# Kernel optimization log

Hardware: AMD Instinct MI355X
Metric: run time of the kernel (lower is better)

The kernel has to match this reference:

```python
import jax, jax.numpy as jnp
import numpy as np

DIM = 512
HEADS = 8
HEAD_DIM = 64
RS = 16        # region_size
EPEG_K = 15
L_TOKENS = 36864  # 192^2, multiple of RS^2 grid


def setup_inputs() -> dict:
    key = jax.random.key(0)
    ks = jax.random.split(key, 5)
    s = 1.0 / np.sqrt(DIM)
    x = jax.random.normal(ks[0], (1, L_TOKENS, DIM), jnp.float32)
    W_qkv = jax.random.normal(ks[1], (3 * HEADS * HEAD_DIM, DIM), jnp.float32) * s
    b_qkv = jnp.zeros((3 * HEADS * HEAD_DIM,), jnp.float32)
    W_proj = jax.random.normal(ks[2], (DIM, HEADS * HEAD_DIM), jnp.float32) * s
    b_proj = jnp.zeros((DIM,), jnp.float32)
    pe_w = jax.random.normal(ks[3], (HEADS, 1, EPEG_K, 1), jnp.float32) * 0.05
    pe_b = jnp.zeros((HEADS,), jnp.float32)
    return dict(x=x, W_qkv=W_qkv, b_qkv=b_qkv, W_proj=W_proj, b_proj=b_proj,
                pe_w=pe_w, pe_b=pe_b)


def reference(x, W_qkv, b_qkv, W_proj, b_proj, pe_w, pe_b):
    B, L, C = x.shape
    # --- padding() logic: square to HxW, H multiple of region_size ---
    H = int(np.ceil(np.sqrt(L)))
    H += (-H) % RS
    W = H
    add = H * W - L
    if add > 0:
        x = jnp.concatenate([x, jnp.zeros((B, add, C), x.dtype)], axis=1)
    # --- region_partition: (B,H,W,C) -> (num_regions*B, RS*RS, C) ---
    xr = (x.reshape(B, H // RS, RS, W // RS, RS, C)
            .transpose(0, 1, 3, 2, 4, 5)
            .reshape(-1, RS * RS, C))
    B_, N, _ = xr.shape
    # --- InnerAttention ---
    qkv = xr @ W_qkv.T + b_qkv                       # (B_, N, 3*h*d)
    qkv = qkv.reshape(B_, N, 3, HEADS, HEAD_DIM).transpose(2, 0, 3, 1, 4)
    q, k, v = qkv[0], qkv[1], qkv[2]                 # each (B_, h, N, d)
    scale = HEAD_DIM ** -0.5
    attn = jnp.einsum('bhid,bhjd->bhij', q * scale, k)   # (B_, h, N, N)
    # EPEG: depthwise conv (k,1) over the query axis of the score map
    pad = EPEG_K // 2
    pe = jax.lax.conv_general_dilated(
        attn, pe_w, window_strides=(1, 1), padding=((pad, pad), (0, 0)),
        dimension_numbers=('NCHW', 'OIHW', 'NCHW'), feature_group_count=HEADS)
    pe = pe + pe_b[None, :, None, None]
    attn = jax.nn.softmax(attn + pe, axis=-1)
    out = jnp.einsum('bhij,bhjd->bhid', attn, v)     # (B_, h, N, d)
    out = out.transpose(0, 2, 1, 3).reshape(B_, N, HEADS * HEAD_DIM)
    out = out @ W_proj.T + b_proj                    # (B_, N, C)
    # --- region_reverse ---
    out = (out.reshape(B, H // RS, W // RS, RS, RS, C)
              .transpose(0, 1, 3, 2, 4, 5)
              .reshape(B, H * W, C))
    if add > 0:
        out = out[:, :L]
    return out
```

## Files before the change

kernel.cpp:

```cpp
#include <hip/hip_runtime.h>
#include <stdint.h>

typedef __attribute__((ext_vector_type(8))) __bf16 bf16x8;
typedef __attribute__((ext_vector_type(16))) float f32x16;

__device__ __forceinline__ unsigned short f2bf(float f) {
  union { float f; unsigned int u; } v;
  v.f = f;
  unsigned int u = v.u;
  return (unsigned short)((u + 0x7FFFu + ((u >> 16) & 1u)) >> 16);
}

union BFrag { unsigned short u[8]; unsigned int w[4]; bf16x8 v; };

__device__ __forceinline__ f32x16 mfma32(bf16x8 a, bf16x8 b, f32x16 c) {
  return __builtin_amdgcn_mfma_f32_32x32x16_bf16(a, b, c, 0, 0, 0);
}

#define GLOAD_LDS16(gptr, lptr)                                                \
  __builtin_amdgcn_global_load_lds(                                           \
      (const __attribute__((address_space(1))) void*)(gptr),                  \
      (__attribute__((address_space(3))) void*)(lptr), 16, 0, 0)

__global__ __launch_bounds__(256) void k_xgather(const float* __restrict__ x,
                                                 unsigned short* __restrict__ xb) {
  int idx = blockIdx.x * 256 + threadIdx.x;
  int m = idx >> 6;
  int seg = (idx & 63) << 3;
  int r = m >> 8, n = m & 255;
  int a = r / 12, b = r - a * 12;
  int ii = n >> 4, jj = n & 15;
  long g = (long)((a * 16 + ii) * 192 + b * 16 + jj);
  const float4* p = (const float4*)(x + g * 512 + seg);
  float4 v0 = p[0], v1 = p[1];
  union { unsigned short u[8]; int4 v; } o;
  o.u[0] = f2bf(v0.x); o.u[1] = f2bf(v0.y); o.u[2] = f2bf(v0.z); o.u[3] = f2bf(v0.w);
  o.u[4] = f2bf(v1.x); o.u[5] = f2bf(v1.y); o.u[6] = f2bf(v1.z); o.u[7] = f2bf(v1.w);
  *(int4*)(xb + (size_t)m * 512 + seg) = o.v;
}

__global__ __launch_bounds__(256) void k_cvt(const float* __restrict__ s,
                                             unsigned short* __restrict__ d, int n8) {
  int i = blockIdx.x * 256 + threadIdx.x;
  if (i >= n8) return;
  const float4* p = (const float4*)(s + (size_t)i * 8);
  float4 a = p[0], b = p[1];
  union { unsigned short u[8]; int4 v; } o;
  o.u[0] = f2bf(a.x); o.u[1] = f2bf(a.y); o.u[2] = f2bf(a.z); o.u[3] = f2bf(a.w);
  o.u[4] = f2bf(b.x); o.u[5] = f2bf(b.y); o.u[6] = f2bf(b.z); o.u[7] = f2bf(b.w);
  *(int4*)(d + (size_t)i * 8) = o.v;
}

template<int MODE, int NBN>
__global__ __launch_bounds__(256, 2) void k_gemm(
    const unsigned short* __restrict__ A, const unsigned short* __restrict__ B,
    const float* __restrict__ bias,
    unsigned short* __restrict__ qb, unsigned short* __restrict__ kb,
    unsigned short* __restrict__ vtb, float* __restrict__ out) {
  __shared__ unsigned short As[8192];
  __shared__ unsigned short Bs[8192];
  int t = threadIdx.x;
  constexpr int NWG = NBN * 288;
  int d0 = blockIdx.x;
  int tl = (d0 & 7) * (NWG >> 3) + (d0 >> 3);
  int bm = tl / NBN, bn = tl % NBN;

  int w = t >> 6, lane = t & 63;
  int l31 = lane & 31, lh = lane >> 5;
  int wr = w >> 1, wc = w & 1;

  int srow = t >> 3, cseg = t & 7;
  int csw = (cseg ^ (srow & 7)) << 3;
  int ldsWaveOff = (t >> 6) << 10;

  f32x16 acc[2][2];
  for (int i = 0; i < 2; ++i)
    for (int j = 0; j < 2; ++j)
      for (int e = 0; e < 16; ++e) acc[i][j][e] = 0.0f;

  const unsigned short* Ag = A + (size_t)(bm * 128 + srow) * 512 + csw;
  const unsigned short* Bg = B + (size_t)(bn * 128 + srow) * 512 + csw;

  for (int ks = 0; ks < 8; ++ks) {
#pragma unroll
    for (int rnd = 0; rnd < 4; ++rnd) {
      GLOAD_LDS16(Ag + (size_t)rnd * 32 * 512 + ks * 64,
                  (char*)As + ldsWaveOff + rnd * 4096);
      GLOAD_LDS16(Bg + (size_t)rnd * 32 * 512 + ks * 64,
                  (char*)Bs + ldsWaveOff + rnd * 4096);
    }
    __syncthreads();
#pragma unroll
    for (int kt = 0; kt < 4; ++kt) {
      bf16x8 af[2], bfr[2];
#pragma unroll
      for (int mt = 0; mt < 2; ++mt) {
        int r = wr * 64 + mt * 32 + l31;
        af[mt] = *(const bf16x8*)((const char*)As + r * 128 +
                                  ((kt * 32 + lh * 16) ^ ((r & 7) << 4)));
      }
#pragma unroll
      for (int nt = 0; nt < 2; ++nt) {
        int r = wc * 64 + nt * 32 + l31;
        bfr[nt] = *(const bf16x8*)((const char*)Bs + r * 128 +
                                   ((kt * 32 + lh * 16) ^ ((r & 7) << 4)));
      }
#pragma unroll
      for (int mt = 0; mt < 2; ++mt)
#pragma unroll
        for (int nt = 0; nt < 2; ++nt)
          acc[mt][nt] = mfma32(af[mt], bfr[nt], acc[mt][nt]);
    }
    __syncthreads();
  }

  int nBase = bn * 128 + wc * 64;
  int mBase = bm * 128 + wr * 64;
#pragma unroll
  for (int nt = 0; nt < 2; ++nt) {
    int nn = nBase + nt * 32 + l31;
    float bs = bias[nn];
    if (MODE == 0) {
      int tsel = nn >> 9, rem = nn & 511;
      int hh = rem >> 6, d = rem & 63;
#pragma unroll
      for (int mt = 0; mt < 2; ++mt) {
#pragma unroll
        for (int q = 0; q < 4; ++q) {
          int m0 = mBase + mt * 32 + q * 8 + lh * 4;
          int r = m0 >> 8, tok = m0 & 255;
          size_t base = (size_t)(r * 8 + hh) * 16384;
          if (tsel == 0) {
#pragma unroll
            for (int j = 0; j < 4; ++j)
              qb[base + (size_t)(tok + j) * 64 + d] = f2bf((acc[mt][nt][q * 4 + j] + bs) * 0.125f);
          } else if (tsel == 1) {
#pragma unroll
            for (int j = 0; j < 4; ++j)
              kb[base + (size_t)(tok + j) * 64 + d] = f2bf(acc[mt][nt][q * 4 + j] + bs);
          } else {
            unsigned long long pv = 0;
#pragma unroll
            for (int j = 0; j < 4; ++j)
              pv |= (unsigned long long)f2bf(acc[mt][nt][q * 4 + j] + bs) << (16 * j);
            *(unsigned long long*)(vtb + base + (size_t)d * 256 + tok) = pv;
          }
        }
      }
    } else {
#pragma unroll
      for (int mt = 0; mt < 2; ++mt) {
#pragma unroll
        for (int q = 0; q < 4; ++q) {
          int m0 = mBase + mt * 32 + q * 8 + lh * 4;
          int r = m0 >> 8;
          int a = r / 12, bcol = r - a * 12;
#pragma unroll
          for (int j = 0; j < 4; ++j) {
            int tok = (m0 & 255) + j;
            int ii = tok >> 4, jj = tok & 15;
            long gg = (long)((a * 16 + ii) * 192 + bcol * 16 + jj);
            out[gg * 512 + nn] = acc[mt][nt][q * 4 + j] + bs;
          }
        }
      }
    }
  }
}

__global__ __launch_bounds__(512, 2) void k_attn12(
    const unsigned short* __restrict__ qb, const unsigned short* __restrict__ kb,
    const unsigned short* __restrict__ vtb, const float* __restrict__ pe_w,
    unsigned short* __restrict__ ctxb) {
  extern __shared__ char lds[];
  int rh = blockIdx.x;
  int h = rh & 7;
  int t = threadIdx.x, w = t >> 6, lane = t & 63;
  int l31 = lane & 31, lh = lane >> 5;
  int iw = w << 5;
  int myi = iw + l31;

  const unsigned short* Qg = qb + (size_t)rh * 16384;
  const unsigned short* Kg = kb + (size_t)rh * 16384;
  const unsigned short* Vg = vtb + (size_t)rh * 16384;
  const float* wh = pe_w + h * 15;

#pragma unroll
  for (int rr = 0; rr < 4; ++rr) {
    int row = rr * 64 + (t >> 3);
    GLOAD_LDS16(Kg + row * 64 + (((t & 7) ^ (row & 7)) << 3), lds + rr * 8192 + t * 16);
  }
  {
    int row = t >> 3;
    GLOAD_LDS16(Vg + row * 256 + (((t & 7) ^ (row & 7)) << 3), lds + 98304 + t * 16);
  }
  if (t < 96) {
    int dlo = t - 40, dhi = t - 39;
    unsigned int lo = (dlo >= 0 && dlo < 15) ? f2bf(wh[dlo]) : 0;
    unsigned int hi = (dhi >= 0 && dhi < 15) ? f2bf(wh[dhi]) : 0;
    *(unsigned int*)(lds + 122880 + t * 4) = lo | (hi << 16);
  }
  bf16x8 qf[4];
#pragma unroll
  for (int kt = 0; kt < 4; ++kt)
    qf[kt] = *(const bf16x8*)(Qg + (size_t)myi * 64 + kt * 16 + lh * 8);
  __syncthreads();

  BFrag band[4];
#pragma unroll
  for (int u = 0; u < 4; ++u) {
    int d0 = 16 * u + 8 * lh - l31 + 31;
#pragma unroll
    for (int e2 = 0; e2 < 4; ++e2)
      band[u].w[e2] = *(const unsigned int*)(lds + 122880 + (d0 + 2 * e2) * 4);
  }

  float m = -3.0e38f, l = 0.0f;
  f32x16 acco[2];
#pragma unroll
  for (int nt = 0; nt < 2; ++nt)
#pragma unroll
    for (int e = 0; e < 16; ++e) acco[nt][e] = 0.0f;

#pragma unroll
  for (int tile = 0; tile < 4; ++tile) {
    char* sbuf = lds + 32768 + (tile & 1) * 32768;
    char* vbuf = lds + 98304 + (tile % 3) * 8192;

    if (tile < 3) {
      int row = t >> 3;
      GLOAD_LDS16(Vg + row * 256 + (tile + 1) * 64 + (((t & 7) ^ (row & 7)) << 3),
                  lds + 98304 + ((tile + 1) % 3) * 8192 + t * 16);
    }

    f32x16 sacc[2];
#pragma unroll
    for (int jb = 0; jb < 2; ++jb)
#pragma unroll
      for (int e = 0; e < 16; ++e) sacc[jb][e] = 0.0f;
#pragma unroll
    for (int jb = 0; jb < 2; ++jb) {
      int kr = tile * 64 + jb * 32 + l31;
#pragma unroll
      for (int kt = 0; kt < 4; ++kt) {
        bf16x8 kf = *(const bf16x8*)(lds + kr * 128 + (((kt * 2 + lh) ^ (kr & 7)) << 4));
        sacc[jb] = mfma32(kf, qf[kt], sacc[jb]);
      }
    }

    {
      int i2 = myi * 2;
#pragma unroll
      for (int jb = 0; jb < 2; ++jb)
#pragma unroll
        for (int rg = 0; rg < 16; ++rg) {
          int j = jb * 32 + (rg & 3) + 8 * (rg >> 2) + 4 * lh;
          *(unsigned short*)(sbuf + j * 512 + (i2 ^ ((j & 7) << 4))) =
              f2bf(sacc[jb][rg]);
        }
    }
    __syncthreads();

#pragma unroll
    for (int jb = 0; jb < 2; ++jb) {
      int jr = jb * 32 + l31;
#pragma unroll
      for (int u = 0; u < 4; ++u) {
        int ktg = 2 * w + u - 1;
        if (ktg >= 0 && ktg < 16) {
          bf16x8 sfr = *(const bf16x8*)(sbuf + jr * 512 +
                                        ((ktg * 32 + lh * 16) ^ ((jr & 7) << 4)));
          sacc[jb] = mfma32(sfr, band[u].v, sacc[jb]);
        }
      }
    }

    float fct;
    {
      float pm = -3.0e38f;
#pragma unroll
      for (int jb = 0; jb < 2; ++jb)
#pragma unroll
        for (int e = 0; e < 16; ++e) pm = fmaxf(pm, sacc[jb][e]);
      pm = fmaxf(pm, __shfl_xor(pm, 32));
      float mn = fmaxf(m, pm);
      float f = __expf(m - mn);
      fct = f;
      float ts = 0.0f;
#pragma unroll
      for (int jb = 0; jb < 2; ++jb)
#pragma unroll
        for (int e = 0; e < 16; ++e) {
          float p = __expf(sacc[jb][e] - mn);
          sacc[jb][e] = p;
          ts += p;
        }
      ts += __shfl_xor(ts, 32);
      l = (tile == 0) ? ts : l * f + ts;
      m = mn;
      if (tile != 0) {
#pragma unroll
        for (int rg = 0; rg < 16; ++rg) {
          float g = __shfl(fct, (rg & 3) + 8 * (rg >> 2) + 4 * lh);
          acco[0][rg] *= g;
          acco[1][rg] *= g;
        }
      }
    }

#pragma unroll
    for (int jb = 0; jb < 2; ++jb) {
      unsigned int pk[8], sw[8];
#pragma unroll
      for (int u = 0; u < 8; ++u)
        pk[u] = (unsigned int)f2bf(sacc[jb][2 * u]) |
                ((unsigned int)f2bf(sacc[jb][2 * u + 1]) << 16);
#pragma unroll
      for (int u = 0; u < 8; ++u) sw[u] = (unsigned int)__shfl_xor((int)pk[u], 32);
      BFrag pf0, pf1;
      if (lh == 0) {
        pf0.w[0] = pk[0]; pf0.w[1] = pk[1]; pf0.w[2] = sw[0]; pf0.w[3] = sw[1];
        pf1.w[0] = pk[4]; pf1.w[1] = pk[5]; pf1.w[2] = sw[4]; pf1.w[3] = sw[5];
      } else {
        pf0.w[0] = sw[2]; pf0.w[1] = sw[3]; pf0.w[2] = pk[2]; pf0.w[3] = pk[3];
        pf1.w[0] = sw[6]; pf1.w[1] = sw[7]; pf1.w[2] = pk[6]; pf1.w[3] = pk[7];
      }
#pragma unroll
      for (int nt = 0; nt < 2; ++nt) {
        int vr = nt * 32 + l31;
        int kj0 = jb * 2;
        bf16x8 vf0 = *(const bf16x8*)(vbuf + vr * 128 +
                                      (((kj0 * 2 + lh) ^ (vr & 7)) << 4));
        bf16x8 vf1 = *(const bf16x8*)(vbuf + vr * 128 +
                                      ((((kj0 + 1) * 2 + lh) ^ (vr & 7)) << 4));
        acco[nt] = mfma32(pf0.v, vf0, acco[nt]);
        acco[nt] = mfma32(pf1.v, vf1, acco[nt]);
      }
    }
  }

  float inv = 1.0f / l;
  int r256 = (rh >> 3) * 256;
  int chbase = h * 64;
#pragma unroll
  for (int rg = 0; rg < 16; ++rg) {
    int cr = (rg & 3) + 8 * (rg >> 2) + 4 * lh;
    float g = __shfl(inv, cr);
    int i = iw + cr;
    size_t rowoff = (size_t)(r256 + i) * 512 + chbase;
    ctxb[rowoff + l31] = f2bf(acco[0][rg] * g);
    ctxb[rowoff + 32 + l31] = f2bf(acco[1][rg] * g);
  }
}

extern "C" void kernel_launch(void* const* d_in, const int* in_sizes, int n_in,
                              void* d_out, int out_size, void* d_ws, size_t ws_size,
                              hipStream_t stream) {
  const float* x = (const float*)d_in[0];
  const float* Wqkv = (const float*)d_in[1];
  const float* bqkv = (const float*)d_in[2];
  const float* Wproj = (const float*)d_in[3];
  const float* bproj = (const float*)d_in[4];
  const float* pew = (const float*)d_in[5];

  char* ws = (char*)d_ws;
  unsigned short* xb = (unsigned short*)ws;
  unsigned short* wqkvb = (unsigned short*)(ws + 37748736);
  unsigned short* wprojb = (unsigned short*)(ws + 39321600);
  unsigned short* qb = (unsigned short*)(ws + 39845888);
  unsigned short* kb = (unsigned short*)(ws + 77594624);
  unsigned short* vtb = (unsigned short*)(ws + 115343360);

  (void)hipFuncSetAttribute((const void*)k_attn12,
                            hipFuncAttributeMaxDynamicSharedMemorySize, 163840);

  k_xgather<<<9216, 256, 0, stream>>>(x, xb);
  k_cvt<<<384, 256, 0, stream>>>(Wqkv, wqkvb, 98304);
  k_cvt<<<128, 256, 0, stream>>>(Wproj, wprojb, 32768);
  k_gemm<0, 12><<<3456, 256, 0, stream>>>(xb, wqkvb, bqkv, qb, kb, vtb, nullptr);
  k_attn12<<<1152, 512, 123264, stream>>>(qb, kb, vtb, pew, xb);
  k_gemm<1, 4><<<1152, 256, 0, stream>>>(xb, wprojb, bproj, nullptr, nullptr, nullptr,
                                         (float*)d_out);
}
```

Before: 219.7 us.

## Use 256x256 GEMM tiles with a four-stage async LDS pipeline

Both GEMMs now use 512-thread blocks computing 256x256 output tiles with a K-step of 32. The LDS loads are issued into a four-buffer ring, prefetching two tiles ahead, and the loop waits with explicit vmcnt instead of a full sync per step. The goal is to hide global-load latency and raise MFMA work per byte loaded. The cost is 128KB of dynamic LDS per block, which limits occupancy to one block per CU. The proj GEMM launches only 288 blocks, which may underfill the 256 CUs and leave a tail.

Result: slower. 246.1 us (+12.0%).

```diff
diff --git a/kernel.cpp b/kernel.cpp
--- a/kernel.cpp
+++ b/kernel.cpp
@@ -52,70 +52,88 @@
 }
 
 template<int MODE, int NBN>
-__global__ __launch_bounds__(256, 2) void k_gemm(
+__global__ __launch_bounds__(512, 2) void k_gemm2(
     const unsigned short* __restrict__ A, const unsigned short* __restrict__ B,
     const float* __restrict__ bias,
     unsigned short* __restrict__ qb, unsigned short* __restrict__ kb,
     unsigned short* __restrict__ vtb, float* __restrict__ out) {
-  __shared__ unsigned short As[8192];
-  __shared__ unsigned short Bs[8192];
+  extern __shared__ char lds[];
   int t = threadIdx.x;
-  constexpr int NWG = NBN * 288;
+  constexpr int NWG = NBN * 144;
   int d0 = blockIdx.x;
   int tl = (d0 & 7) * (NWG >> 3) + (d0 >> 3);
   int bm = tl / NBN, bn = tl % NBN;
 
   int w = t >> 6, lane = t & 63;
   int l31 = lane & 31, lh = lane >> 5;
-  int wr = w >> 1, wc = w & 1;
-
-  int srow = t >> 3, cseg = t & 7;
-  int csw = (cseg ^ (srow & 7)) << 3;
-  int ldsWaveOff = (t >> 6) << 10;
-
-  f32x16 acc[2][2];
-  for (int i = 0; i < 2; ++i)
+  int wr = w >> 2, wc = w & 3;
+
+  int srow = t >> 2, sseg = t & 3;
+
+  f32x16 acc[4][2];
+#pragma unroll
+  for (int i = 0; i < 4; ++i)
+#pragma unroll
     for (int j = 0; j < 2; ++j)
+#pragma unroll
       for (int e = 0; e < 16; ++e) acc[i][j][e] = 0.0f;
 
-  const unsigned short* Ag = A + (size_t)(bm * 128 + srow) * 512 + csw;
-  const unsigned short* Bg = B + (size_t)(bn * 128 + srow) * 512 + csw;
-
-  for (int ks = 0; ks < 8; ++ks) {
-#pragma unroll
-    for (int rnd = 0; rnd < 4; ++rnd) {
-      GLOAD_LDS16(Ag + (size_t)rnd * 32 * 512 + ks * 64,
-                  (char*)As + ldsWaveOff + rnd * 4096);
-      GLOAD_LDS16(Bg + (size_t)rnd * 32 * 512 + ks * 64,
-                  (char*)Bs + ldsWaveOff + rnd * 4096);
-    }
-    __syncthreads();
-#pragma unroll
-    for (int kt = 0; kt < 4; ++kt) {
-      bf16x8 af[2], bfr[2];
-#pragma unroll
-      for (int mt = 0; mt < 2; ++mt) {
-        int r = wr * 64 + mt * 32 + l31;
-        af[mt] = *(const bf16x8*)((const char*)As + r * 128 +
-                                  ((kt * 32 + lh * 16) ^ ((r & 7) << 4)));
+  const unsigned short* Ag0 = A + (size_t)(bm * 256) * 512;
+  const unsigned short* Bg0 = B + (size_t)(bn * 256) * 512;
+
+#define STAGE2(tile)                                                           \
+  {                                                                            \
+    char* buf_ = lds + ((tile) & 3) * 32768;                                   \
+    _Pragma("unroll")                                                          \
+    for (int r_ = 0; r_ < 2; ++r_) {                                           \
+      int row_ = r_ * 128 + srow;                                              \
+      int csw_ = (sseg ^ (row_ & 3)) << 3;                                     \
+      GLOAD_LDS16(Ag0 + (size_t)row_ * 512 + (tile) * 32 + csw_,               \
+                  buf_ + r_ * 8192 + t * 16);                                  \
+      GLOAD_LDS16(Bg0 + (size_t)row_ * 512 + (tile) * 32 + csw_,               \
+                  buf_ + 16384 + r_ * 8192 + t * 16);                          \
+    }                                                                          \
+  }
+
+  STAGE2(0);
+  STAGE2(1);
+  asm volatile("s_waitcnt vmcnt(4)" ::: "memory");
+  __builtin_amdgcn_s_barrier();
+
+#pragma unroll
+  for (int kt0 = 0; kt0 < 16; ++kt0) {
+    if (kt0 < 14) STAGE2(kt0 + 2);
+    const char* abuf = lds + (kt0 & 3) * 32768;
+    const char* bbuf = abuf + 16384;
+#pragma unroll
+    for (int kt = 0; kt < 2; ++kt) {
+      bf16x8 af[4], bfr[2];
+#pragma unroll
+      for (int mt = 0; mt < 4; ++mt) {
+        int r = wr * 128 + mt * 32 + l31;
+        af[mt] = *(const bf16x8*)(abuf + r * 64 + (((kt * 2 + lh) ^ (r & 3)) << 4));
       }
 #pragma unroll
       for (int nt = 0; nt < 2; ++nt) {
         int r = wc * 64 + nt * 32 + l31;
-        bfr[nt] = *(const bf16x8*)((const char*)Bs + r * 128 +
-                                   ((kt * 32 + lh * 16) ^ ((r & 7) << 4)));
-      }
-#pragma unroll
-      for (int mt = 0; mt < 2; ++mt)
+        bfr[nt] = *(const bf16x8*)(bbuf + r * 64 + (((kt * 2 + lh) ^ (r & 3)) << 4));
+      }
+#pragma unroll
+      for (int mt = 0; mt < 4; ++mt)
 #pragma unroll
         for (int nt = 0; nt < 2; ++nt)
           acc[mt][nt] = mfma32(af[mt], bfr[nt], acc[mt][nt]);
     }
-    __syncthreads();
-  }
-
-  int nBase = bn * 128 + wc * 64;
-  int mBase = bm * 128 + wr * 64;
+    if (kt0 < 14) {
+      asm volatile("s_waitcnt vmcnt(4)" ::: "memory");
+    } else if (kt0 == 14) {
+      asm volatile("s_waitcnt vmcnt(0)" ::: "memory");
+    }
+    if (kt0 < 15) __builtin_amdgcn_s_barrier();
+  }
+
+  int nBase = bn * 256 + wc * 64;
+  int mBase = bm * 256 + wr * 128;
 #pragma unroll
   for (int nt = 0; nt < 2; ++nt) {
     int nn = nBase + nt * 32 + l31;
@@ -124,7 +142,7 @@
       int tsel = nn >> 9, rem = nn & 511;
       int hh = rem >> 6, d = rem & 63;
 #pragma unroll
-      for (int mt = 0; mt < 2; ++mt) {
+      for (int mt = 0; mt < 4; ++mt) {
 #pragma unroll
         for (int q = 0; q < 4; ++q) {
           int m0 = mBase + mt * 32 + q * 8 + lh * 4;
@@ -149,7 +167,7 @@
       }
     } else {
 #pragma unroll
-      for (int mt = 0; mt < 2; ++mt) {
+      for (int mt = 0; mt < 4; ++mt) {
 #pragma unroll
         for (int q = 0; q < 4; ++q) {
           int m0 = mBase + mt * 32 + q * 8 + lh * 4;
@@ -373,12 +391,16 @@
 
   (void)hipFuncSetAttribute((const void*)k_attn12,
                             hipFuncAttributeMaxDynamicSharedMemorySize, 163840);
+  (void)hipFuncSetAttribute((const void*)k_gemm2<0, 6>,
+                            hipFuncAttributeMaxDynamicSharedMemorySize, 131072);
+  (void)hipFuncSetAttribute((const void*)k_gemm2<1, 2>,
+                            hipFuncAttributeMaxDynamicSharedMemorySize, 131072);
 
   k_xgather<<<9216, 256, 0, stream>>>(x, xb);
   k_cvt<<<384, 256, 0, stream>>>(Wqkv, wqkvb, 98304);
   k_cvt<<<128, 256, 0, stream>>>(Wproj, wprojb, 32768);
-  k_gemm<0, 12><<<3456, 256, 0, stream>>>(xb, wqkvb, bqkv, qb, kb, vtb, nullptr);
+  k_gemm2<0, 6><<<864, 512, 131072, stream>>>(xb, wqkvb, bqkv, qb, kb, vtb, nullptr);
   k_attn12<<<1152, 512, 123264, stream>>>(qb, kb, vtb, pew, xb);
-  k_gemm<1, 4><<<1152, 256, 0, stream>>>(xb, wprojb, bproj, nullptr, nullptr, nullptr,
-                                         (float*)d_out);
-}
+  k_gemm2<1, 2><<<288, 512, 131072, stream>>>(xb, wprojb, bproj, nullptr, nullptr, nullptr,
+                                              (float*)d_out);
+}
```
